# Performance work log

Measured on AMD Instinct MI355X. Metric: run time of the kernel, lower is better.

Reference implementation:

```python
import jax, jax.numpy as jnp
import numpy as np

NUM_EMBEDDINGS = 1024
EMBEDDING_DIM = 256
COMMITMENT_COST = 0.25
TEMPERATURE = 0.05


def setup_inputs() -> dict:
    key = jax.random.key(0)
    kz, ke = jax.random.split(key)
    z = jax.random.normal(kz, (32, 1024, EMBEDDING_DIM), dtype=jnp.float32)
    # nn.init.uniform_(weight, -1/num_embeddings, 1/num_embeddings)
    lim = 1.0 / NUM_EMBEDDINGS
    emb = jax.random.uniform(ke, (NUM_EMBEDDINGS, EMBEDDING_DIM), dtype=jnp.float32,
                             minval=-lim, maxval=lim)
    return {"z": z, "emb": emb}


def reference(z, emb):
    B, T, D = z.shape
    flat_z = z.reshape(-1, D)  # (N, D)
    # squared euclidean distances: (N, K)
    distances = (jnp.sum(flat_z ** 2, axis=1, keepdims=True)
                 + jnp.sum(emb ** 2, axis=1)
                 - 2.0 * flat_z @ emb.T)
    soft_probs = jax.nn.softmax(-distances / TEMPERATURE, axis=1)  # (N, K)
    avg_soft_probs = soft_probs.mean(axis=0)  # (K,)
    encoding_indices = jnp.argmin(distances, axis=1)  # (N,)
    # one-hot @ codebook == gather
    quantized = emb[encoding_indices].reshape(B, T, D)
    e_latent_loss = jnp.mean((jax.lax.stop_gradient(quantized) - z) ** 2)
    q_latent_loss = jnp.mean((quantized - jax.lax.stop_gradient(z)) ** 2)
    vq_loss = q_latent_loss + COMMITMENT_COST * e_latent_loss
    # straight-through estimator
    quantized_st = z + jax.lax.stop_gradient(quantized - z)
    return (quantized_st, vq_loss, encoding_indices.reshape(B, T), avg_soft_probs)
```

## Files before the change

kernel.cpp:

```cpp
#include <hip/hip_runtime.h>
#include <hip/hip_bf16.h>

#define N_ROWS   32768
#define DIM      256
#define DIM4     64
#define K_CODES  1024
#define INV_T    20.0f
#define SCREEN_W 4e-4f

#define LOSS_OFF 8388608
#define IDX_OFF  8388609
#define AVG_OFF  8421377

typedef float  f32x4  __attribute__((ext_vector_type(4)));
typedef short  short8 __attribute__((ext_vector_type(8)));
typedef unsigned long long u64;

static __device__ __forceinline__ unsigned short f2bf(float x) {
    union { __hip_bfloat16 b; unsigned short u; } v;
    v.b = __float2bfloat16(x);
    return v.u;
}
static __device__ __forceinline__ float bf2f(unsigned short h) {
    union { unsigned int u; float f; } v;
    v.u = ((unsigned int)h) << 16;
    return v.f;
}

__global__ void vq_norms(const float* __restrict__ emb, float* __restrict__ ne) {
    int k = blockIdx.x * blockDim.x + threadIdx.x;
    if (k >= K_CODES) return;
    const float* row = emb + (size_t)k * DIM;
    float blk[2];
    #pragma unroll
    for (int b = 0; b < 2; ++b) {
        const float* x = row + b * 128;
        float r[8];
        #pragma unroll
        for (int j = 0; j < 8; ++j) r[j] = __fmul_rn(x[j], x[j]);
        for (int i = 8; i < 128; i += 8) {
            #pragma unroll
            for (int j = 0; j < 8; ++j)
                r[j] = __fadd_rn(r[j], __fmul_rn(x[i + j], x[i + j]));
        }
        float t01 = __fadd_rn(r[0], r[1]);
        float t23 = __fadd_rn(r[2], r[3]);
        float t45 = __fadd_rn(r[4], r[5]);
        float t67 = __fadd_rn(r[6], r[7]);
        blk[b] = __fadd_rn(__fadd_rn(t01, t23), __fadd_rn(t45, t67));
    }
    ne[k] = __fadd_rn(blk[0], blk[1]);
}

__global__ void vq_init(float* __restrict__ out) {
    int i = blockIdx.x * blockDim.x + threadIdx.x;
    if (i == 0) out[LOSS_OFF] = 0.f;
    if (i < K_CODES) out[AVG_OFF + i] = 0.f;
}

__global__ __launch_bounds__(256) void vq_main(
    const float4* __restrict__ z4,
    const float4* __restrict__ emb4,
    const float* __restrict__ ne,
    float* __restrict__ out)
{
    __shared__ __align__(16) char uni[32768];
    __shared__ __align__(16) unsigned short zhs[8192];
    __shared__ __align__(16) unsigned short zls[8192];
    __shared__ float avg_lds[K_CODES];
    __shared__ float nzs[32];
    __shared__ float rowmin2[32][2];
    __shared__ float rowsum2[32][2];
    __shared__ u64   rowwin[32];
    __shared__ unsigned int list[512];
    __shared__ int   listCount;
    __shared__ float redbuf[4];

    const int t    = threadIdx.x;
    const int n0   = blockIdx.x * 32;
    const int lane = t & 63;
    const int w    = t >> 6;
    const int rt   = w & 1;
    const int ch   = w >> 1;

    #pragma unroll
    for (int i = 0; i < 4; ++i) avg_lds[i * 256 + t] = 0.f;
    if (t < 32) rowwin[t] = ~0ull;
    if (t == 0) listCount = 0;

    float* zs = reinterpret_cast<float*>(uni);
    #pragma unroll
    for (int i = 0; i < 8; ++i) {
        int f = i * 256 + t;
        reinterpret_cast<float4*>(zs)[f] = z4[(size_t)n0 * DIM4 + f];
    }
    __syncthreads();

    {
        const int j8   = lane & 7;
        const int blk  = (lane >> 3) & 1;
        const int rsub = lane >> 4;
        #pragma unroll
        for (int p = 0; p < 2; ++p) {
            int row = p * 16 + w * 4 + rsub;
            const float* x = zs + row * 256 + blk * 128;
            float v0 = x[j8];
            float s = __fmul_rn(v0, v0);
            #pragma unroll
            for (int b = 1; b < 16; ++b) {
                float v = x[j8 + 8 * b];
                s = __fadd_rn(s, __fmul_rn(v, v));
            }
            s = __fadd_rn(s, __shfl_xor(s, 1));
            s = __fadd_rn(s, __shfl_xor(s, 2));
            s = __fadd_rn(s, __shfl_xor(s, 4));
            s = __fadd_rn(s, __shfl_xor(s, 8));
            if ((lane & 15) == 0) nzs[row] = s;
        }
    }

    #pragma unroll
    for (int i = 0; i < 32; ++i) {
        int f = i * 256 + t;
        int row = f >> 8, d = f & 255;
        float zv = zs[f];
        unsigned short h = f2bf(zv);
        unsigned short l = f2bf(zv - bf2f(h));
        int colb = (d * 2) ^ ((row & 7) << 4);
        *reinterpret_cast<unsigned short*>(reinterpret_cast<char*>(zhs) + row * 512 + colb) = h;
        *reinterpret_cast<unsigned short*>(reinterpret_cast<char*>(zls) + row * 512 + colb) = l;
    }
    __syncthreads();

    const int arow = rt * 16 + (lane & 15);
    const int hi16 = (lane >> 4) * 16;
    const int swzr = (arow & 7) << 4;
    const char* zhb = reinterpret_cast<const char*>(zhs) + arow * 512;
    const char* zlb = reinterpret_cast<const char*>(zls) + arow * 512;
    short8 azh[8];
    #pragma unroll
    for (int k = 0; k < 8; ++k)
        azh[k] = *reinterpret_cast<const short8*>(zhb + ((k * 64 + hi16) ^ swzr));

    f32x4 acc[32];
    #pragma unroll
    for (int i = 0; i < 32; ++i) acc[i] = (f32x4){0.f, 0.f, 0.f, 0.f};

    const int bc    = lane & 15;
    const int swzc  = (bc & 7) << 4;
    const char* ebase = uni + ch * 16384 + bc * 512;

    #pragma unroll
    for (int it = 0; it < 32; ++it) {
        #pragma unroll
        for (int i = 0; i < 8; ++i) {
            int f = i * 256 + t;
            int cr = f >> 6, d4 = f & 63;
            int half = cr >> 4, c = cr & 15;
            int gcode = half * 512 + it * 16 + c;
            float4 e4 = emb4[(size_t)gcode * DIM4 + d4];
            ushort4 h4, l4;
            h4.x = f2bf(e4.x); l4.x = f2bf(e4.x - bf2f(h4.x));
            h4.y = f2bf(e4.y); l4.y = f2bf(e4.y - bf2f(h4.y));
            h4.z = f2bf(e4.z); l4.z = f2bf(e4.z - bf2f(h4.z));
            h4.w = f2bf(e4.w); l4.w = f2bf(e4.w - bf2f(h4.w));
            char* base = uni + half * 16384 + c * 512;
            int kbs = (d4 * 8) ^ ((c & 7) << 4);
            *reinterpret_cast<ushort4*>(base + kbs) = h4;
            *reinterpret_cast<ushort4*>(base + 8192 + kbs) = l4;
        }
        __syncthreads();

        #pragma unroll
        for (int k = 0; k < 8; ++k) {
            int off = (k * 64 + hi16) ^ swzc;
            short8 ebh = *reinterpret_cast<const short8*>(ebase + off);
            short8 ebl = *reinterpret_cast<const short8*>(ebase + 8192 + off);
            short8 azl = *reinterpret_cast<const short8*>(zlb + ((k * 64 + hi16) ^ swzr));
            acc[it] = __builtin_amdgcn_mfma_f32_16x16x32_bf16(azh[k], ebh, acc[it], 0, 0, 0);
            acc[it] = __builtin_amdgcn_mfma_f32_16x16x32_bf16(azh[k], ebl, acc[it], 0, 0, 0);
            acc[it] = __builtin_amdgcn_mfma_f32_16x16x32_bf16(azl,    ebh, acc[it], 0, 0, 0);
        }
        __syncthreads();
    }

    const int lrow0 = rt * 16 + (lane >> 4) * 4;
    float nzv[4];
    #pragma unroll
    for (int r = 0; r < 4; ++r) nzv[r] = nzs[lrow0 + r];

    #pragma unroll
    for (int it = 0; it < 32; ++it) {
        int code = ch * 512 + it * 16 + (lane & 15);
        float nev = ne[code];
        #pragma unroll
        for (int r = 0; r < 4; ++r)
            acc[it][r] = (nzv[r] + nev) - 2.f * acc[it][r];
    }

    float mn[4] = {3.4e38f, 3.4e38f, 3.4e38f, 3.4e38f};
    #pragma unroll
    for (int it = 0; it < 32; ++it) {
        #pragma unroll
        for (int r = 0; r < 4; ++r) mn[r] = fminf(mn[r], acc[it][r]);
    }
    #pragma unroll
    for (int r = 0; r < 4; ++r) {
        mn[r] = fminf(mn[r], __shfl_xor(mn[r], 1));
        mn[r] = fminf(mn[r], __shfl_xor(mn[r], 2));
        mn[r] = fminf(mn[r], __shfl_xor(mn[r], 4));
        mn[r] = fminf(mn[r], __shfl_xor(mn[r], 8));
    }
    if ((lane & 15) == 0) {
        #pragma unroll
        for (int r = 0; r < 4; ++r) rowmin2[lrow0 + r][ch] = mn[r];
    }
    __syncthreads();
    float rmn[4];
    #pragma unroll
    for (int r = 0; r < 4; ++r)
        rmn[r] = fminf(rowmin2[lrow0 + r][0], rowmin2[lrow0 + r][1]);

    #pragma unroll
    for (int it = 0; it < 32; ++it) {
        int code = ch * 512 + it * 16 + (lane & 15);
        #pragma unroll
        for (int r = 0; r < 4; ++r) {
            if (acc[it][r] <= rmn[r] + SCREEN_W) {
                int idx = atomicAdd(&listCount, 1);
                if (idx < 512) list[idx] = ((unsigned int)(lrow0 + r) << 10) | (unsigned int)code;
            }
        }
    }

    float sm[4] = {0.f, 0.f, 0.f, 0.f};
    #pragma unroll
    for (int it = 0; it < 32; ++it) {
        #pragma unroll
        for (int r = 0; r < 4; ++r) {
            float u = __expf((rmn[r] - acc[it][r]) * INV_T);
            acc[it][r] = u;
            sm[r] += u;
        }
    }
    #pragma unroll
    for (int r = 0; r < 4; ++r) {
        sm[r] += __shfl_xor(sm[r], 1);
        sm[r] += __shfl_xor(sm[r], 2);
        sm[r] += __shfl_xor(sm[r], 4);
        sm[r] += __shfl_xor(sm[r], 8);
    }
    if ((lane & 15) == 0) {
        #pragma unroll
        for (int r = 0; r < 4; ++r) rowsum2[lrow0 + r][ch] = sm[r];
    }
    __syncthreads();

    float inv[4];
    #pragma unroll
    for (int r = 0; r < 4; ++r)
        inv[r] = 1.f / (rowsum2[lrow0 + r][0] + rowsum2[lrow0 + r][1]);

    #pragma unroll
    for (int it = 0; it < 32; ++it) {
        float pit = acc[it][0] * inv[0] + acc[it][1] * inv[1]
                  + acc[it][2] * inv[2] + acc[it][3] * inv[3];
        pit += __shfl_xor(pit, 16);
        pit += __shfl_xor(pit, 32);
        if (lane < 16)
            atomicAdd(&avg_lds[ch * 512 + it * 16 + lane], pit);
    }

    {
        int cnt = listCount; if (cnt > 512) cnt = 512;
        for (int i = t; i < cnt; i += 256) {
            unsigned int p = list[i];
            int lrow = (int)(p >> 10);
            int code = (int)(p & 1023u);
            const float4* zr = z4 + (size_t)(n0 + lrow) * DIM4;
            const float4* er = emb4 + (size_t)code * DIM4;
            float a0 = 0.f;
            for (int d4 = 0; d4 < DIM4; ++d4) {
                float4 v = zr[d4];
                float4 e = er[d4];
                a0 = __builtin_fmaf(v.x, e.x, a0);
                a0 = __builtin_fmaf(v.y, e.y, a0);
                a0 = __builtin_fmaf(v.z, e.z, a0);
                a0 = __builtin_fmaf(v.w, e.w, a0);
            }
            float S = __fadd_rn(nzs[lrow], ne[code]);
            float d = __fsub_rn(S, 2.f * a0);
            u64 key = ((u64)__float_as_uint(d) << 32) | (u64)(unsigned int)code;
            atomicMin(&rowwin[lrow], key);
        }
    }
    __syncthreads();

    #pragma unroll
    for (int i = 0; i < 4; ++i) {
        int k = i * 256 + t;
        atomicAdd(&out[AVG_OFF + k], avg_lds[k] * (1.0f / (float)N_ROWS));
    }
    if (t < 32)
        out[IDX_OFF + n0 + t] = (float)(unsigned int)(rowwin[t] & 0xFFFFFFFFull);

    float lpart = 0.f;
    #pragma unroll
    for (int i = 0; i < 8; ++i) {
        int f = i * 256 + t;
        int r = f >> 6, d4 = f & 63;
        int bi = (int)(unsigned int)(rowwin[r] & 0xFFFFFFFFull);
        float4 q = emb4[(size_t)bi * DIM4 + d4];
        reinterpret_cast<float4*>(out)[(size_t)(n0 + r) * DIM4 + d4] = q;
        float4 zz = z4[(size_t)(n0 + r) * DIM4 + d4];
        float dx = q.x - zz.x, dy = q.y - zz.y, dz = q.z - zz.z, dw = q.w - zz.w;
        lpart += dx * dx + dy * dy + dz * dz + dw * dw;
    }
    #pragma unroll
    for (int off = 32; off >= 1; off >>= 1) lpart += __shfl_xor(lpart, off);
    if ((t & 63) == 0) redbuf[t >> 6] = lpart;
    __syncthreads();
    if (t == 0) {
        float tot = redbuf[0] + redbuf[1] + redbuf[2] + redbuf[3];
        atomicAdd(&out[LOSS_OFF], tot * (1.25f / (float)(N_ROWS * DIM)));
    }
}

extern "C" void kernel_launch(void* const* d_in, const int* in_sizes, int n_in,
                              void* d_out, int out_size, void* d_ws, size_t ws_size,
                              hipStream_t stream) {
    const float* z   = (const float*)d_in[0];
    const float* emb = (const float*)d_in[1];
    float* out = (float*)d_out;
    float* ne  = (float*)d_ws;

    vq_norms<<<dim3(4), dim3(256), 0, stream>>>(emb, ne);
    vq_init<<<dim3(4), dim3(256), 0, stream>>>(out);
    vq_main<<<dim3(N_ROWS / 32), dim3(256), 0, stream>>>(
        (const float4*)z, (const float4*)emb, ne, out);
}
```

Before: 328.2 us.

## Drop split-bf16 correction MFMAs, use single bf16 GEMM with fragment-order LDS layout

Replaces the three-MFMA split-bf16 emulation (hi*hi, hi*lo, lo*hi) with a single bf16 MFMA per tile, cutting matrix work and LDS traffic to about a third. Z and codebook tiles are now written to LDS directly in MFMA fragment order (no swizzle), and each stage loads 32 codes per half so two accumulators share one A fragment. To keep argmin exact under the lower-precision distances, the screening window is widened and the candidate list doubled, and candidates are rescored in fp32. The risk is more candidates to rescore and softmax probabilities computed from less accurate bf16 distances.

```diff
diff --git a/kernel.cpp b/kernel.cpp
--- a/kernel.cpp
+++ b/kernel.cpp
@@ -6,25 +6,21 @@
 #define DIM4     64
 #define K_CODES  1024
 #define INV_T    20.0f
-#define SCREEN_W 4e-4f
+#define SCREEN_W 5e-4f
 
 #define LOSS_OFF 8388608
 #define IDX_OFF  8388609
 #define AVG_OFF  8421377
 
-typedef float  f32x4  __attribute__((ext_vector_type(4)));
-typedef short  short8 __attribute__((ext_vector_type(8)));
+typedef float  f32x4   __attribute__((ext_vector_type(4)));
+typedef short  short8  __attribute__((ext_vector_type(8)));
+typedef unsigned short ushort8 __attribute__((ext_vector_type(8)));
 typedef unsigned long long u64;
 
 static __device__ __forceinline__ unsigned short f2bf(float x) {
     union { __hip_bfloat16 b; unsigned short u; } v;
     v.b = __float2bfloat16(x);
     return v.u;
-}
-static __device__ __forceinline__ float bf2f(unsigned short h) {
-    union { unsigned int u; float f; } v;
-    v.u = ((unsigned int)h) << 16;
-    return v.f;
 }
 
 __global__ void vq_norms(const float* __restrict__ emb, float* __restrict__ ne) {
@@ -65,14 +61,13 @@
     float* __restrict__ out)
 {
     __shared__ __align__(16) char uni[32768];
-    __shared__ __align__(16) unsigned short zhs[8192];
-    __shared__ __align__(16) unsigned short zls[8192];
+    __shared__ __align__(16) char zh_lds[16384];
     __shared__ float avg_lds[K_CODES];
     __shared__ float nzs[32];
     __shared__ float rowmin2[32][2];
     __shared__ float rowsum2[32][2];
     __shared__ u64   rowwin[32];
-    __shared__ unsigned int list[512];
+    __shared__ unsigned int list[1024];
     __shared__ int   listCount;
     __shared__ float redbuf[4];
 
@@ -120,89 +115,81 @@
     }
 
     #pragma unroll
-    for (int i = 0; i < 32; ++i) {
-        int f = i * 256 + t;
-        int row = f >> 8, d = f & 255;
-        float zv = zs[f];
-        unsigned short h = f2bf(zv);
-        unsigned short l = f2bf(zv - bf2f(h));
-        int colb = (d * 2) ^ ((row & 7) << 4);
-        *reinterpret_cast<unsigned short*>(reinterpret_cast<char*>(zhs) + row * 512 + colb) = h;
-        *reinterpret_cast<unsigned short*>(reinterpret_cast<char*>(zls) + row * 512 + colb) = l;
-    }
-    __syncthreads();
-
-    const int arow = rt * 16 + (lane & 15);
-    const int hi16 = (lane >> 4) * 16;
-    const int swzr = (arow & 7) << 4;
-    const char* zhb = reinterpret_cast<const char*>(zhs) + arow * 512;
-    const char* zlb = reinterpret_cast<const char*>(zls) + arow * 512;
-    short8 azh[8];
-    #pragma unroll
-    for (int k = 0; k < 8; ++k)
-        azh[k] = *reinterpret_cast<const short8*>(zhb + ((k * 64 + hi16) ^ swzr));
+    for (int i = 0; i < 4; ++i) {
+        int fl  = i * 256 + t;
+        int r   = fl & 15;
+        int q   = (fl >> 4) & 3;
+        int k   = (fl >> 6) & 7;
+        int rt2 = fl >> 9;
+        int f40 = (n0 + rt2 * 16 + r) * DIM4 + k * 8 + q * 2;
+        float4 za = z4[f40];
+        float4 zb = z4[f40 + 1];
+        ushort8 v;
+        v[0] = f2bf(za.x); v[1] = f2bf(za.y); v[2] = f2bf(za.z); v[3] = f2bf(za.w);
+        v[4] = f2bf(zb.x); v[5] = f2bf(zb.y); v[6] = f2bf(zb.z); v[7] = f2bf(zb.w);
+        *reinterpret_cast<ushort8*>(zh_lds + fl * 16) = v;
+    }
+    __syncthreads();
 
     f32x4 acc[32];
     #pragma unroll
     for (int i = 0; i < 32; ++i) acc[i] = (f32x4){0.f, 0.f, 0.f, 0.f};
 
+    const char* Abase = zh_lds + rt * 8192;
+    const char* Bbase = uni + ch * 16384;
+
+    #pragma unroll
+    for (int it = 0; it < 16; ++it) {
+        #pragma unroll
+        for (int i = 0; i < 8; ++i) {
+            int fl   = i * 256 + t;
+            int bc   = fl & 15;
+            int q    = (fl >> 4) & 3;
+            int k    = (fl >> 6) & 7;
+            int ct   = (fl >> 9) & 1;
+            int half = fl >> 10;
+            int gcode = half * 512 + it * 32 + ct * 16 + bc;
+            int f40 = gcode * DIM4 + k * 8 + q * 2;
+            float4 ea = emb4[f40];
+            float4 eb = emb4[f40 + 1];
+            ushort8 v;
+            v[0] = f2bf(ea.x); v[1] = f2bf(ea.y); v[2] = f2bf(ea.z); v[3] = f2bf(ea.w);
+            v[4] = f2bf(eb.x); v[5] = f2bf(eb.y); v[6] = f2bf(eb.z); v[7] = f2bf(eb.w);
+            *reinterpret_cast<ushort8*>(uni + fl * 16) = v;
+        }
+        __syncthreads();
+
+        #pragma unroll
+        for (int k = 0; k < 8; ++k) {
+            short8 A  = *reinterpret_cast<const short8*>(Abase + k * 1024 + lane * 16);
+            short8 B0 = *reinterpret_cast<const short8*>(Bbase + k * 1024 + lane * 16);
+            short8 B1 = *reinterpret_cast<const short8*>(Bbase + 8192 + k * 1024 + lane * 16);
+            acc[it * 2]     = __builtin_amdgcn_mfma_f32_16x16x32_bf16(A, B0, acc[it * 2], 0, 0, 0);
+            acc[it * 2 + 1] = __builtin_amdgcn_mfma_f32_16x16x32_bf16(A, B1, acc[it * 2 + 1], 0, 0, 0);
+        }
+        __syncthreads();
+    }
+
     const int bc    = lane & 15;
-    const int swzc  = (bc & 7) << 4;
-    const char* ebase = uni + ch * 16384 + bc * 512;
-
-    #pragma unroll
-    for (int it = 0; it < 32; ++it) {
-        #pragma unroll
-        for (int i = 0; i < 8; ++i) {
-            int f = i * 256 + t;
-            int cr = f >> 6, d4 = f & 63;
-            int half = cr >> 4, c = cr & 15;
-            int gcode = half * 512 + it * 16 + c;
-            float4 e4 = emb4[(size_t)gcode * DIM4 + d4];
-            ushort4 h4, l4;
-            h4.x = f2bf(e4.x); l4.x = f2bf(e4.x - bf2f(h4.x));
-            h4.y = f2bf(e4.y); l4.y = f2bf(e4.y - bf2f(h4.y));
-            h4.z = f2bf(e4.z); l4.z = f2bf(e4.z - bf2f(h4.z));
-            h4.w = f2bf(e4.w); l4.w = f2bf(e4.w - bf2f(h4.w));
-            char* base = uni + half * 16384 + c * 512;
-            int kbs = (d4 * 8) ^ ((c & 7) << 4);
-            *reinterpret_cast<ushort4*>(base + kbs) = h4;
-            *reinterpret_cast<ushort4*>(base + 8192 + kbs) = l4;
-        }
-        __syncthreads();
-
-        #pragma unroll
-        for (int k = 0; k < 8; ++k) {
-            int off = (k * 64 + hi16) ^ swzc;
-            short8 ebh = *reinterpret_cast<const short8*>(ebase + off);
-            short8 ebl = *reinterpret_cast<const short8*>(ebase + 8192 + off);
-            short8 azl = *reinterpret_cast<const short8*>(zlb + ((k * 64 + hi16) ^ swzr));
-            acc[it] = __builtin_amdgcn_mfma_f32_16x16x32_bf16(azh[k], ebh, acc[it], 0, 0, 0);
-            acc[it] = __builtin_amdgcn_mfma_f32_16x16x32_bf16(azh[k], ebl, acc[it], 0, 0, 0);
-            acc[it] = __builtin_amdgcn_mfma_f32_16x16x32_bf16(azl,    ebh, acc[it], 0, 0, 0);
-        }
-        __syncthreads();
-    }
-
     const int lrow0 = rt * 16 + (lane >> 4) * 4;
     float nzv[4];
     #pragma unroll
     for (int r = 0; r < 4; ++r) nzv[r] = nzs[lrow0 + r];
 
     #pragma unroll
-    for (int it = 0; it < 32; ++it) {
-        int code = ch * 512 + it * 16 + (lane & 15);
+    for (int j = 0; j < 32; ++j) {
+        int code = ch * 512 + (j >> 1) * 32 + (j & 1) * 16 + bc;
         float nev = ne[code];
         #pragma unroll
         for (int r = 0; r < 4; ++r)
-            acc[it][r] = (nzv[r] + nev) - 2.f * acc[it][r];
+            acc[j][r] = (nzv[r] + nev) - 2.f * acc[j][r];
     }
 
     float mn[4] = {3.4e38f, 3.4e38f, 3.4e38f, 3.4e38f};
     #pragma unroll
-    for (int it = 0; it < 32; ++it) {
-        #pragma unroll
-        for (int r = 0; r < 4; ++r) mn[r] = fminf(mn[r], acc[it][r]);
+    for (int j = 0; j < 32; ++j) {
+        #pragma unroll
+        for (int r = 0; r < 4; ++r) mn[r] = fminf(mn[r], acc[j][r]);
     }
     #pragma unroll
     for (int r = 0; r < 4; ++r) {
@@ -222,24 +209,24 @@
         rmn[r] = fminf(rowmin2[lrow0 + r][0], rowmin2[lrow0 + r][1]);
 
     #pragma unroll
-    for (int it = 0; it < 32; ++it) {
-        int code = ch * 512 + it * 16 + (lane & 15);
+    for (int j = 0; j < 32; ++j) {
+        int code = ch * 512 + (j >> 1) * 32 + (j & 1) * 16 + bc;
         #pragma unroll
         for (int r = 0; r < 4; ++r) {
-            if (acc[it][r] <= rmn[r] + SCREEN_W) {
+            if (acc[j][r] <= rmn[r] + SCREEN_W) {
                 int idx = atomicAdd(&listCount, 1);
-                if (idx < 512) list[idx] = ((unsigned int)(lrow0 + r) << 10) | (unsigned int)code;
+                if (idx < 1024) list[idx] = ((unsigned int)(lrow0 + r) << 10) | (unsigned int)code;
             }
         }
     }
 
     float sm[4] = {0.f, 0.f, 0.f, 0.f};
     #pragma unroll
-    for (int it = 0; it < 32; ++it) {
+    for (int j = 0; j < 32; ++j) {
         #pragma unroll
         for (int r = 0; r < 4; ++r) {
-            float u = __expf((rmn[r] - acc[it][r]) * INV_T);
-            acc[it][r] = u;
+            float u = __expf((rmn[r] - acc[j][r]) * INV_T);
+            acc[j][r] = u;
             sm[r] += u;
         }
     }
@@ -262,17 +249,17 @@
         inv[r] = 1.f / (rowsum2[lrow0 + r][0] + rowsum2[lrow0 + r][1]);
 
     #pragma unroll
-    for (int it = 0; it < 32; ++it) {
-        float pit = acc[it][0] * inv[0] + acc[it][1] * inv[1]
-                  + acc[it][2] * inv[2] + acc[it][3] * inv[3];
+    for (int j = 0; j < 32; ++j) {
+        float pit = acc[j][0] * inv[0] + acc[j][1] * inv[1]
+                  + acc[j][2] * inv[2] + acc[j][3] * inv[3];
         pit += __shfl_xor(pit, 16);
         pit += __shfl_xor(pit, 32);
         if (lane < 16)
-            atomicAdd(&avg_lds[ch * 512 + it * 16 + lane], pit);
+            atomicAdd(&avg_lds[ch * 512 + (j >> 1) * 32 + (j & 1) * 16 + lane], pit);
     }
 
     {
-        int cnt = listCount; if (cnt > 512) cnt = 512;
+        int cnt = listCount; if (cnt > 1024) cnt = 1024;
         for (int i = t; i < cnt; i += 256) {
             unsigned int p = list[i];
             int lrow = (int)(p >> 10);
```

Result: faster. 317.7 us (-3.2%).
